# Kernel tuning notes

Hardware: AMD Instinct MI355X
Metric: run time of the kernel (lower is better)

## Reference

```python
import jax, jax.numpy as jnp
import numpy as np

B, S, H, NH = 2, 2048, 1024, 16
HD = H // NH  # head_dim = 64


def setup_inputs() -> dict:
    key = jax.random.key(0)
    kx, kl, kq, kk, kv, ko = jax.random.split(key, 6)
    scale = 1.0 / np.sqrt(H)
    return {
        "x": jax.random.normal(kx, (B, S, H), dtype=jnp.float32),
        "seq_lengths": jax.random.randint(kl, (B,), 1, S + 1, dtype=jnp.int32),
        "Wq": jax.random.normal(kq, (H, H), dtype=jnp.float32) * scale,
        "Wk": jax.random.normal(kk, (H, H), dtype=jnp.float32) * scale,
        "Wv": jax.random.normal(kv, (H, H), dtype=jnp.float32) * scale,
        "Wo": jax.random.normal(ko, (H, H), dtype=jnp.float32) * scale,
    }


def reference(x, seq_lengths, Wq, Wk, Wv, Wo):
    b, s, _ = x.shape
    # projections (nn.Linear with no bias: x @ W.T)
    q = (x @ Wq.T).reshape(b, s, NH, HD).transpose(0, 2, 1, 3)  # [b,h,s,d]
    k = (x @ Wk.T).reshape(b, s, NH, HD).transpose(0, 2, 1, 3)
    v = (x @ Wv.T).reshape(b, s, NH, HD).transpose(0, 2, 1, 3)

    scores = jnp.einsum("bhqd,bhkd->bhqk", q, k) / jnp.sqrt(jnp.float32(HD))

    causal = jnp.triu(jnp.ones((s, s), dtype=bool), k=1)[None, None]  # [1,1,s,s]
    padding = (jnp.arange(s)[None, :] >= seq_lengths[:, None])[:, None, None, :]
    mask = causal | padding
    scores = jnp.where(mask, -jnp.inf, scores)

    att = jax.nn.softmax(scores, axis=-1)  # stable: subtract row max once
    out = jnp.einsum("bhqk,bhkd->bhqd", att, v)
    out = out.transpose(0, 2, 1, 3).reshape(b, s, H)
    return out @ Wo.T
```

## Files before the change

### kernel.cpp

```cpp
#include <hip/hip_runtime.h>

typedef unsigned short u16;
typedef short bf16x8 __attribute__((ext_vector_type(8)));
typedef float f32x4 __attribute__((ext_vector_type(4)));

#define DEVINL __device__ __forceinline__

DEVINL u16 f2bf(float f) {
    union { float f; unsigned int u; } x;
    x.f = f;
    unsigned int u = x.u;
    unsigned int r = (u + 0x7fffu + ((u >> 16) & 1u)) >> 16;
    return (u16)r;
}

DEVINL u16 f2bf_fast(float f) {
    union { float f; unsigned int u; } x;
    x.f = f;
    return (u16)((x.u + 0x8000u) >> 16);
}

DEVINL void async16(const u16* g, u16* l) {
    __builtin_amdgcn_global_load_lds(
        (const __attribute__((address_space(1))) void*)g,
        (__attribute__((address_space(3))) void*)l, 16, 0, 0);
}

DEVINL void store_out(u16* p, float v)   { *p = f2bf(v); }
DEVINL void store_out(float* p, float v) { *p = v; }

__global__ void pma_cvt_kernel(const float* __restrict__ in, u16* __restrict__ out, int n4) {
    int i = blockIdx.x * blockDim.x + threadIdx.x;
    if (i < n4) {
        float4 v = reinterpret_cast<const float4*>(in)[i];
        ushort4 o;
        o.x = f2bf(v.x); o.y = f2bf(v.y); o.z = f2bf(v.z); o.w = f2bf(v.w);
        reinterpret_cast<ushort4*>(out)[i] = o;
    }
}

__global__ void pma_cvt4_kernel(const float* __restrict__ w0, const float* __restrict__ w1,
                                const float* __restrict__ w2, const float* __restrict__ w3,
                                u16* __restrict__ dst) {
    const int wsel = blockIdx.y;
    const float* in = (wsel == 0) ? w0 : (wsel == 1) ? w1 : (wsel == 2) ? w2 : w3;
    u16* out = dst + (size_t)wsel * 1024 * 1024;
    const float s = (wsel == 0) ? 0.125f : 1.0f;
    int i = blockIdx.x * blockDim.x + threadIdx.x;
    float4 v = reinterpret_cast<const float4*>(in)[i];
    ushort4 o;
    o.x = f2bf(v.x * s); o.y = f2bf(v.y * s); o.z = f2bf(v.z * s); o.w = f2bf(v.w * s);
    reinterpret_cast<ushort4*>(out)[i] = o;
}

template <typename OutT>
__global__ __launch_bounds__(256) void pma_gemm_bt(
    const u16* __restrict__ A,
    const u16* __restrict__ W0, const u16* __restrict__ W1, const u16* __restrict__ W2,
    OutT* __restrict__ O0, OutT* __restrict__ O1, OutT* __restrict__ O2,
    int K, int nbn_per, int vtr_which,
    const int* __restrict__ seq_lengths, int skip_kv)
{
    const int t = threadIdx.x;
    const int lane = t & 63, wave = t >> 6;
    const int m0 = blockIdx.x * 128;
    const int bn = blockIdx.y;
    const int which = bn / nbn_per;
    const int n0 = (bn % nbn_per) * 128;

    if (skip_kv && which != 0) {
        if ((m0 & 2047) >= seq_lengths[m0 >> 11]) return;
    }

    const u16* W = (which == 0) ? W0 : (which == 1) ? W1 : W2;
    OutT* O = (which == 0) ? O0 : (which == 1) ? O1 : O2;

    __shared__ u16 Alds[128 * 32];
    __shared__ u16 Blds[128 * 32];

    const int wm = wave >> 1, wn = wave & 1;
    const int r16 = lane & 15, g4 = lane >> 4;

    f32x4 acc[4][4];
    const f32x4 z = {0.f, 0.f, 0.f, 0.f};
#pragma unroll
    for (int m = 0; m < 4; ++m)
#pragma unroll
        for (int n = 0; n < 4; ++n) acc[m][n] = z;

    for (int k0 = 0; k0 < K; k0 += 32) {
        __syncthreads();
#pragma unroll
        for (int j = 0; j < 2; ++j) {
            int i = j * 256 + t;
            int row = i >> 2, seg = i & 3;
            async16(A + (size_t)(m0 + row) * K + k0 + seg * 8,
                    Alds + (size_t)(j * 256 + wave * 64) * 8);
            async16(W + (size_t)(n0 + row) * K + k0 + seg * 8,
                    Blds + (size_t)(j * 256 + wave * 64) * 8);
        }
        __syncthreads();

        bf16x8 af[4], bfr[4];
#pragma unroll
        for (int m = 0; m < 4; ++m)
            af[m] = *reinterpret_cast<const bf16x8*>(Alds + (wm * 64 + m * 16 + r16) * 32 + g4 * 8);
#pragma unroll
        for (int n = 0; n < 4; ++n)
            bfr[n] = *reinterpret_cast<const bf16x8*>(Blds + (wn * 64 + n * 16 + r16) * 32 + g4 * 8);
#pragma unroll
        for (int m = 0; m < 4; ++m)
#pragma unroll
            for (int n = 0; n < 4; ++n)
                acc[m][n] = __builtin_amdgcn_mfma_f32_16x16x32_bf16(af[m], bfr[n], acc[m][n], 0, 0, 0);
    }

    bool vtr = false;
    if constexpr (sizeof(OutT) == 2) vtr = (which == vtr_which);
    if (vtr) {
        if constexpr (sizeof(OutT) == 2) {
#pragma unroll
            for (int m = 0; m < 4; ++m)
#pragma unroll
                for (int n = 0; n < 4; ++n) {
                    int row = m0 + wm * 64 + m * 16 + g4 * 4;
                    int col = n0 + wn * 64 + n * 16 + r16;
                    ushort4 pk;
                    pk.x = f2bf(acc[m][n][0]); pk.y = f2bf(acc[m][n][1]);
                    pk.z = f2bf(acc[m][n][2]); pk.w = f2bf(acc[m][n][3]);
                    size_t addr = ((size_t)((row >> 11) * 16 + (col >> 6)) * 64 + (col & 63)) * 2048
                                  + (row & 2047);
                    *reinterpret_cast<ushort4*>((u16*)O + addr) = pk;
                }
        }
    } else {
#pragma unroll
        for (int m = 0; m < 4; ++m)
#pragma unroll
            for (int n = 0; n < 4; ++n) {
                int row = m0 + wm * 64 + m * 16 + g4 * 4;
                int col = n0 + wn * 64 + n * 16 + r16;
#pragma unroll
                for (int r = 0; r < 4; ++r)
                    store_out(&O[(size_t)(row + r) * 1024 + col], acc[m][n][r]);
            }
    }
}

__global__ __launch_bounds__(256, 4) void pma_attn_kernel(
    const u16* __restrict__ Q, const u16* __restrict__ Kp, const u16* __restrict__ Vt,
    const int* __restrict__ seq_lengths, u16* __restrict__ O)
{
    const int bx = blockIdx.x;
    const int qt = 31 - (bx >> 5);
    const int bh = bx & 31;
    const int h  = bh & 15;
    const int b  = bh >> 4;
    const int q0 = qt * 64;
    const int t = threadIdx.x, lane = t & 63, w = t >> 6;
    const int r16 = lane & 15, g4 = lane >> 4;
    const int seqlen = seq_lengths[b];
    const float L2E = 1.4426950408889634f;

    __shared__ u16 Klds[2 * 64 * 64];
    __shared__ u16 Vlds[2 * 64 * 64];
    __shared__ u16 Plds[64 * 64];

    const size_t bbase = (size_t)b * 2048 * 1024;
    const size_t hoff = (size_t)h * 64;
    const size_t vrow0 = (size_t)((b * 16 + h) * 64);

    const f32x4 z = {0.f, 0.f, 0.f, 0.f};
    const int krel = t >> 3;
    const int seg  = t & 7;

    const size_t qrowbase = bbase + (size_t)(q0 + w * 16 + r16) * 1024 + hoff;
    const bf16x8 qf0 = *reinterpret_cast<const bf16x8*>(Q + qrowbase + g4 * 8);
    const bf16x8 qf1 = *reinterpret_cast<const bf16x8*>(Q + qrowbase + 32 + g4 * 8);

    f32x4 acc[4];
#pragma unroll
    for (int f = 0; f < 4; ++f) acc[f] = z;
    float mrow = -1e30f, lrow = 0.f;

    int kmax = q0 + 63;
    if (seqlen - 1 < kmax) kmax = seqlen - 1;
    const int nt = (kmax >> 6) + 1;

    const u16* kbase = Kp + bbase + hoff + (size_t)krel * 1024 + seg * 8;
    const u16* vbase = Vt + (vrow0 + krel) * 2048 + seg * 8;
    const int stw = krel * 64 + ((seg ^ (krel & 7)) * 8);

    const int r7 = r16 & 7;
    const int kread_lo = r16 * 64 + ((g4 ^ r7) * 8);
    const int kread_hi = r16 * 64 + (((g4 + 4) ^ r7) * 8);
    const int prow = (w * 16 + r16) * 64;

    bf16x8 kreg[2], vreg[2];

#pragma unroll
    for (int j = 0; j < 2; ++j) {
        kreg[j] = *reinterpret_cast<const bf16x8*>(kbase + j * 32 * 1024);
        vreg[j] = *reinterpret_cast<const bf16x8*>(vbase + j * 32 * 2048);
    }
#pragma unroll
    for (int j = 0; j < 2; ++j) {
        *reinterpret_cast<bf16x8*>(Klds + stw + j * 2048) = kreg[j];
        *reinterpret_cast<bf16x8*>(Vlds + stw + j * 2048) = vreg[j];
    }
    __syncthreads();

    const int qhat = q0 + w * 16 + r16;

    for (int tt = 0; tt < nt; ++tt) {
        const int t0 = tt << 6;
        const int dbo = (tt & 1) << 12;
        const int dbn = 4096 - dbo;

        if (tt + 1 < nt) {
            const int t0n = (tt + 1) << 6;
#pragma unroll
            for (int j = 0; j < 2; ++j) {
                kreg[j] = *reinterpret_cast<const bf16x8*>(kbase + (size_t)t0n * 1024 + j * 32 * 1024);
                vreg[j] = *reinterpret_cast<const bf16x8*>(vbase + t0n + j * 32 * 2048);
            }
        }

        f32x4 sraw[4];
        __builtin_amdgcn_s_setprio(1);
#pragma unroll
        for (int kc = 0; kc < 4; ++kc) {
            bf16x8 kf0 = *reinterpret_cast<const bf16x8*>(Klds + dbo + kc * 1024 + kread_lo);
            bf16x8 kf1 = *reinterpret_cast<const bf16x8*>(Klds + dbo + kc * 1024 + kread_hi);
            f32x4 s = z;
            s = __builtin_amdgcn_mfma_f32_16x16x32_bf16(kf0, qf0, s, 0, 0, 0);
            s = __builtin_amdgcn_mfma_f32_16x16x32_bf16(kf1, qf1, s, 0, 0, 0);
            sraw[kc] = s;
        }
        __builtin_amdgcn_s_setprio(0);

        float sc[4][4];
        const bool needmask = (t0 == q0) || (t0 + 64 > seqlen);
        if (needmask) {
#pragma unroll
            for (int kc = 0; kc < 4; ++kc) {
                const int keyb = t0 + kc * 16 + g4 * 4;
#pragma unroll
                for (int r = 0; r < 4; ++r)
                    sc[kc][r] = ((keyb + r > qhat) || (keyb + r >= seqlen)) ? -1e30f : sraw[kc][r];
            }
        } else {
#pragma unroll
            for (int kc = 0; kc < 4; ++kc)
#pragma unroll
                for (int r = 0; r < 4; ++r) sc[kc][r] = sraw[kc][r];
        }

        float mx;
        {
            float m0 = fmaxf(fmaxf(sc[0][0], sc[0][1]), fmaxf(sc[0][2], sc[0][3]));
            float m1 = fmaxf(fmaxf(sc[1][0], sc[1][1]), fmaxf(sc[1][2], sc[1][3]));
            float m2 = fmaxf(fmaxf(sc[2][0], sc[2][1]), fmaxf(sc[2][2], sc[2][3]));
            float m3 = fmaxf(fmaxf(sc[3][0], sc[3][1]), fmaxf(sc[3][2], sc[3][3]));
            mx = fmaxf(fmaxf(m0, m1), fmaxf(m2, m3));
        }
        mx = fmaxf(mx, __shfl_xor(mx, 16, 64));
        mx = fmaxf(mx, __shfl_xor(mx, 32, 64));

        const bool norescale = __all(mx <= mrow + 8.0f);
        float mnew, corr;
        if (norescale) { mnew = mrow; corr = 1.0f; }
        else           { mnew = fmaxf(mrow, mx); corr = exp2f((mrow - mnew) * L2E); }

        const float nb = mnew * L2E;
#pragma unroll
        for (int kc = 0; kc < 4; ++kc)
#pragma unroll
            for (int r = 0; r < 4; ++r)
                sc[kc][r] = exp2f(__builtin_fmaf(sc[kc][r], L2E, -nb));
        float rs;
        {
            float s0 = (sc[0][0] + sc[0][1]) + (sc[0][2] + sc[0][3]);
            float s1 = (sc[1][0] + sc[1][1]) + (sc[1][2] + sc[1][3]);
            float s2 = (sc[2][0] + sc[2][1]) + (sc[2][2] + sc[2][3]);
            float s3 = (sc[3][0] + sc[3][1]) + (sc[3][2] + sc[3][3]);
            rs = (s0 + s1) + (s2 + s3);
        }
        rs += __shfl_xor(rs, 16, 64);
        rs += __shfl_xor(rs, 32, 64);
        lrow = lrow * corr + rs;
        mrow = mnew;

#pragma unroll
        for (int kc = 0; kc < 4; ++kc) {
            ushort4 pk;
            pk.x = f2bf_fast(sc[kc][0]); pk.y = f2bf_fast(sc[kc][1]);
            pk.z = f2bf_fast(sc[kc][2]); pk.w = f2bf_fast(sc[kc][3]);
            const int phys16 = (kc * 2 + (g4 >> 1)) ^ r7;
            *reinterpret_cast<ushort4*>(Plds + prow + phys16 * 8 + (g4 & 1) * 4) = pk;
        }

        if (!norescale) {
            float cr0 = __shfl(corr, g4 * 4 + 0, 64);
            float cr1 = __shfl(corr, g4 * 4 + 1, 64);
            float cr2 = __shfl(corr, g4 * 4 + 2, 64);
            float cr3 = __shfl(corr, g4 * 4 + 3, 64);
#pragma unroll
            for (int f = 0; f < 4; ++f) {
                f32x4 a = acc[f];
                a[0] *= cr0; a[1] *= cr1; a[2] *= cr2; a[3] *= cr3;
                acc[f] = a;
            }
        }

        __builtin_amdgcn_s_setprio(1);
#pragma unroll
        for (int kc2 = 0; kc2 < 2; ++kc2) {
            bf16x8 pa = *reinterpret_cast<const bf16x8*>(Plds + prow + (((kc2 * 4 + g4) ^ r7) * 8));
#pragma unroll
            for (int f = 0; f < 4; ++f) {
                bf16x8 vb = *reinterpret_cast<const bf16x8*>(
                    Vlds + dbo + (f * 16 + r16) * 64 + (((kc2 * 4 + g4) ^ r7) * 8));
                acc[f] = __builtin_amdgcn_mfma_f32_16x16x32_bf16(pa, vb, acc[f], 0, 0, 0);
            }
        }
        __builtin_amdgcn_s_setprio(0);

        if (tt + 1 < nt) {
#pragma unroll
            for (int j = 0; j < 2; ++j) {
                *reinterpret_cast<bf16x8*>(Klds + dbn + stw + j * 2048) = kreg[j];
                *reinterpret_cast<bf16x8*>(Vlds + dbn + stw + j * 2048) = vreg[j];
            }
            __syncthreads();
        }
    }

    {
        float lr0 = __shfl(lrow, g4 * 4 + 0, 64);
        float lr1 = __shfl(lrow, g4 * 4 + 1, 64);
        float lr2 = __shfl(lrow, g4 * 4 + 2, 64);
        float lr3 = __shfl(lrow, g4 * 4 + 3, 64);
        float lr[4] = {lr0, lr1, lr2, lr3};
#pragma unroll
        for (int f = 0; f < 4; ++f)
#pragma unroll
            for (int r = 0; r < 4; ++r) {
                int sr = q0 + w * 16 + g4 * 4 + r;
                float o = acc[f][r] / lr[r];
                O[bbase + (size_t)sr * 1024 + hoff + f * 16 + r16] = f2bf(o);
            }
    }
}

extern "C" void kernel_launch(void* const* d_in, const int* in_sizes, int n_in,
                              void* d_out, int out_size, void* d_ws, size_t ws_size,
                              hipStream_t stream) {
    const float* x   = (const float*)d_in[0];
    const int*   sql = (const int*)d_in[1];
    const float* Wq  = (const float*)d_in[2];
    const float* Wk  = (const float*)d_in[3];
    const float* Wv  = (const float*)d_in[4];
    const float* Wo  = (const float*)d_in[5];
    float* out = (float*)d_out;

    const size_t MB = 1024 * 1024;
    char* ws = (char*)d_ws;
    u16* xb   = (u16*)(ws + 0 * MB);
    u16* wqb  = (u16*)(ws + 8 * MB);
    u16* wkb  = (u16*)(ws + 10 * MB);
    u16* wvb  = (u16*)(ws + 12 * MB);
    u16* wob  = (u16*)(ws + 14 * MB);
    u16* Qb   = (u16*)(ws + 16 * MB);
    u16* Kb   = (u16*)(ws + 24 * MB);
    u16* Vtb  = (u16*)(ws + 32 * MB);
    u16* attb = (u16*)(ws + 40 * MB);

    pma_cvt_kernel<<<4096, 256, 0, stream>>>(x, xb, 1048576);
    pma_cvt4_kernel<<<dim3(1024, 4), 256, 0, stream>>>(Wq, Wk, Wv, Wo, wqb);

    pma_gemm_bt<u16><<<dim3(32, 24), 256, 0, stream>>>(xb, wqb, wkb, wvb, Qb, Kb, Vtb,
                                                       1024, 8, 2, sql, 1);

    pma_attn_kernel<<<1024, 256, 0, stream>>>(Qb, Kb, Vtb, sql, attb);

    pma_gemm_bt<float><<<dim3(32, 8), 256, 0, stream>>>(attb, wob, wob, wob, out, out, out,
                                                        1024, 8, -1, sql, 0);
}
```

Before: 120.8 us.

## Split GEMM into specialized QKV and output kernels with swizzled K=64 tiles

New measurement: 121.6 us. No clear change (+0.7%).

```diff
diff --git a/kernel.cpp b/kernel.cpp
--- a/kernel.cpp
+++ b/kernel.cpp
@@ -26,8 +26,9 @@
         (__attribute__((address_space(3))) void*)l, 16, 0, 0);
 }
 
-DEVINL void store_out(u16* p, float v)   { *p = f2bf(v); }
-DEVINL void store_out(float* p, float v) { *p = v; }
+DEVINL f32x4 mfma32(bf16x8 a, bf16x8 b, f32x4 c) {
+    return __builtin_amdgcn_mfma_f32_16x16x32_bf16(a, b, c, 0, 0, 0);
+}
 
 __global__ void pma_cvt_kernel(const float* __restrict__ in, u16* __restrict__ out, int n4) {
     int i = blockIdx.x * blockDim.x + threadIdx.x;
@@ -53,33 +54,29 @@
     reinterpret_cast<ushort4*>(out)[i] = o;
 }
 
-template <typename OutT>
-__global__ __launch_bounds__(256) void pma_gemm_bt(
+__global__ __launch_bounds__(256) void pma_gemm_qkv(
     const u16* __restrict__ A,
     const u16* __restrict__ W0, const u16* __restrict__ W1, const u16* __restrict__ W2,
-    OutT* __restrict__ O0, OutT* __restrict__ O1, OutT* __restrict__ O2,
-    int K, int nbn_per, int vtr_which,
-    const int* __restrict__ seq_lengths, int skip_kv)
+    u16* __restrict__ O0, u16* __restrict__ O1, u16* __restrict__ Vt,
+    const int* __restrict__ seq_lengths)
 {
     const int t = threadIdx.x;
     const int lane = t & 63, wave = t >> 6;
     const int m0 = blockIdx.x * 128;
     const int bn = blockIdx.y;
-    const int which = bn / nbn_per;
-    const int n0 = (bn % nbn_per) * 128;
-
-    if (skip_kv && which != 0) {
-        if ((m0 & 2047) >= seq_lengths[m0 >> 11]) return;
-    }
+    const int which = bn >> 3;
+    const int n0 = (bn & 7) * 128;
+
+    if (which != 0 && (m0 & 2047) >= seq_lengths[m0 >> 11]) return;
 
     const u16* W = (which == 0) ? W0 : (which == 1) ? W1 : W2;
-    OutT* O = (which == 0) ? O0 : (which == 1) ? O1 : O2;
-
-    __shared__ u16 Alds[128 * 32];
-    __shared__ u16 Blds[128 * 32];
+
+    __shared__ u16 Alds[128 * 64];
+    __shared__ u16 Blds[128 * 64];
 
     const int wm = wave >> 1, wn = wave & 1;
     const int r16 = lane & 15, g4 = lane >> 4;
+    const int r7 = r16 & 7;
 
     f32x4 acc[4][4];
     const f32x4 z = {0.f, 0.f, 0.f, 0.f};
@@ -88,63 +85,128 @@
 #pragma unroll
         for (int n = 0; n < 4; ++n) acc[m][n] = z;
 
-    for (int k0 = 0; k0 < K; k0 += 32) {
+    for (int k0 = 0; k0 < 1024; k0 += 64) {
         __syncthreads();
+#pragma unroll
+        for (int j = 0; j < 4; ++j) {
+            int i = j * 256 + t;
+            int row = i >> 3, seg = i & 7;
+            int sc = ((seg ^ (row & 7)) * 8);
+            async16(A + (size_t)(m0 + row) * 1024 + k0 + sc,
+                    Alds + (size_t)(j * 256 + wave * 64) * 8);
+            async16(W + (size_t)(n0 + row) * 1024 + k0 + sc,
+                    Blds + (size_t)(j * 256 + wave * 64) * 8);
+        }
+        __syncthreads();
+
+#pragma unroll
+        for (int half = 0; half < 2; ++half) {
+            bf16x8 af[4], bfr[4];
+#pragma unroll
+            for (int m = 0; m < 4; ++m)
+                af[m] = *reinterpret_cast<const bf16x8*>(
+                    Alds + (wm * 64 + m * 16 + r16) * 64 + (((half * 4 + g4) ^ r7) * 8));
+#pragma unroll
+            for (int n = 0; n < 4; ++n)
+                bfr[n] = *reinterpret_cast<const bf16x8*>(
+                    Blds + (wn * 64 + n * 16 + r16) * 64 + (((half * 4 + g4) ^ r7) * 8));
+#pragma unroll
+            for (int m = 0; m < 4; ++m)
+#pragma unroll
+                for (int n = 0; n < 4; ++n)
+                    acc[m][n] = mfma32(af[m], bfr[n], acc[m][n]);
+        }
+    }
+
+    if (which == 2) {
+#pragma unroll
+        for (int m = 0; m < 4; ++m)
+#pragma unroll
+            for (int n = 0; n < 4; ++n) {
+                int row = m0 + wm * 64 + m * 16 + g4 * 4;
+                int col = n0 + wn * 64 + n * 16 + r16;
+                ushort4 pk;
+                pk.x = f2bf(acc[m][n][0]); pk.y = f2bf(acc[m][n][1]);
+                pk.z = f2bf(acc[m][n][2]); pk.w = f2bf(acc[m][n][3]);
+                size_t addr = ((size_t)((row >> 11) * 16 + (col >> 6)) * 64 + (col & 63)) * 2048
+                              + (row & 2047);
+                *reinterpret_cast<ushort4*>(Vt + addr) = pk;
+            }
+    } else {
+        u16* O = (which == 0) ? O0 : O1;
+#pragma unroll
+        for (int m = 0; m < 4; ++m)
+#pragma unroll
+            for (int n = 0; n < 4; ++n) {
+                int row = m0 + wm * 64 + m * 16 + g4 * 4;
+                int col = n0 + wn * 64 + n * 16 + r16;
+#pragma unroll
+                for (int r = 0; r < 4; ++r)
+                    O[(size_t)(row + r) * 1024 + col] = f2bf(acc[m][n][r]);
+            }
+    }
+}
+
+__global__ __launch_bounds__(256) void pma_gemm_wo(
+    const u16* __restrict__ A, const u16* __restrict__ W, float* __restrict__ O)
+{
+    const int t = threadIdx.x;
+    const int lane = t & 63, wave = t >> 6;
+    const int m0 = blockIdx.x * 64;
+    const int n0 = blockIdx.y * 128;
+
+    __shared__ u16 Alds[64 * 32];
+    __shared__ u16 Blds[128 * 32];
+
+    const int r16 = lane & 15, g4 = lane >> 4;
+
+    f32x4 acc[4][2];
+    const f32x4 z = {0.f, 0.f, 0.f, 0.f};
+#pragma unroll
+    for (int m = 0; m < 4; ++m) {
+        acc[m][0] = z; acc[m][1] = z;
+    }
+
+    for (int k0 = 0; k0 < 1024; k0 += 32) {
+        __syncthreads();
+        {
+            int row = t >> 2, seg = t & 3;
+            async16(A + (size_t)(m0 + row) * 1024 + k0 + seg * 8,
+                    Alds + (size_t)(wave * 64) * 8);
+        }
 #pragma unroll
         for (int j = 0; j < 2; ++j) {
             int i = j * 256 + t;
             int row = i >> 2, seg = i & 3;
-            async16(A + (size_t)(m0 + row) * K + k0 + seg * 8,
-                    Alds + (size_t)(j * 256 + wave * 64) * 8);
-            async16(W + (size_t)(n0 + row) * K + k0 + seg * 8,
+            async16(W + (size_t)(n0 + row) * 1024 + k0 + seg * 8,
                     Blds + (size_t)(j * 256 + wave * 64) * 8);
         }
         __syncthreads();
 
-        bf16x8 af[4], bfr[4];
+        bf16x8 af[4], bfr[2];
 #pragma unroll
         for (int m = 0; m < 4; ++m)
-            af[m] = *reinterpret_cast<const bf16x8*>(Alds + (wm * 64 + m * 16 + r16) * 32 + g4 * 8);
-#pragma unroll
-        for (int n = 0; n < 4; ++n)
-            bfr[n] = *reinterpret_cast<const bf16x8*>(Blds + (wn * 64 + n * 16 + r16) * 32 + g4 * 8);
+            af[m] = *reinterpret_cast<const bf16x8*>(Alds + (m * 16 + r16) * 32 + g4 * 8);
+#pragma unroll
+        for (int n = 0; n < 2; ++n)
+            bfr[n] = *reinterpret_cast<const bf16x8*>(Blds + (wave * 32 + n * 16 + r16) * 32 + g4 * 8);
 #pragma unroll
         for (int m = 0; m < 4; ++m)
 #pragma unroll
-            for (int n = 0; n < 4; ++n)
-                acc[m][n] = __builtin_amdgcn_mfma_f32_16x16x32_bf16(af[m], bfr[n], acc[m][n], 0, 0, 0);
-    }
-
-    bool vtr = false;
-    if constexpr (sizeof(OutT) == 2) vtr = (which == vtr_which);
-    if (vtr) {
-        if constexpr (sizeof(OutT) == 2) {
-#pragma unroll
-            for (int m = 0; m < 4; ++m)
-#pragma unroll
-                for (int n = 0; n < 4; ++n) {
-                    int row = m0 + wm * 64 + m * 16 + g4 * 4;
-                    int col = n0 + wn * 64 + n * 16 + r16;
-                    ushort4 pk;
-                    pk.x = f2bf(acc[m][n][0]); pk.y = f2bf(acc[m][n][1]);
-                    pk.z = f2bf(acc[m][n][2]); pk.w = f2bf(acc[m][n][3]);
-                    size_t addr = ((size_t)((row >> 11) * 16 + (col >> 6)) * 64 + (col & 63)) * 2048
-                                  + (row & 2047);
-                    *reinterpret_cast<ushort4*>((u16*)O + addr) = pk;
-                }
-        }
-    } else {
-#pragma unroll
-        for (int m = 0; m < 4; ++m)
-#pragma unroll
-            for (int n = 0; n < 4; ++n) {
-                int row = m0 + wm * 64 + m * 16 + g4 * 4;
-                int col = n0 + wn * 64 + n * 16 + r16;
-#pragma unroll
-                for (int r = 0; r < 4; ++r)
-                    store_out(&O[(size_t)(row + r) * 1024 + col], acc[m][n][r]);
-            }
-    }
+            for (int n = 0; n < 2; ++n)
+                acc[m][n] = mfma32(af[m], bfr[n], acc[m][n]);
+    }
+
+#pragma unroll
+    for (int m = 0; m < 4; ++m)
+#pragma unroll
+        for (int n = 0; n < 2; ++n) {
+            int row = m0 + m * 16 + g4 * 4;
+            int col = n0 + wave * 32 + n * 16 + r16;
+#pragma unroll
+            for (int r = 0; r < 4; ++r)
+                O[(size_t)(row + r) * 1024 + col] = acc[m][n][r];
+        }
 }
 
 __global__ __launch_bounds__(256, 4) void pma_attn_kernel(
@@ -233,8 +295,8 @@
             bf16x8 kf0 = *reinterpret_cast<const bf16x8*>(Klds + dbo + kc * 1024 + kread_lo);
             bf16x8 kf1 = *reinterpret_cast<const bf16x8*>(Klds + dbo + kc * 1024 + kread_hi);
             f32x4 s = z;
-            s = __builtin_amdgcn_mfma_f32_16x16x32_bf16(kf0, qf0, s, 0, 0, 0);
-            s = __builtin_amdgcn_mfma_f32_16x16x32_bf16(kf1, qf1, s, 0, 0, 0);
+            s = mfma32(kf0, qf0, s);
+            s = mfma32(kf1, qf1, s);
             sraw[kc] = s;
         }
         __builtin_amdgcn_s_setprio(0);
@@ -321,7 +383,7 @@
             for (int f = 0; f < 4; ++f) {
                 bf16x8 vb = *reinterpret_cast<const bf16x8*>(
                     Vlds + dbo + (f * 16 + r16) * 64 + (((kc2 * 4 + g4) ^ r7) * 8));
-                acc[f] = __builtin_amdgcn_mfma_f32_16x16x32_bf16(pa, vb, acc[f], 0, 0, 0);
+                acc[f] = mfma32(pa, vb, acc[f]);
             }
         }
         __builtin_amdgcn_s_setprio(0);
@@ -379,11 +441,9 @@
     pma_cvt_kernel<<<4096, 256, 0, stream>>>(x, xb, 1048576);
     pma_cvt4_kernel<<<dim3(1024, 4), 256, 0, stream>>>(Wq, Wk, Wv, Wo, wqb);
 
-    pma_gemm_bt<u16><<<dim3(32, 24), 256, 0, stream>>>(xb, wqb, wkb, wvb, Qb, Kb, Vtb,
-                                                       1024, 8, 2, sql, 1);
+    pma_gemm_qkv<<<dim3(32, 24), 256, 0, stream>>>(xb, wqb, wkb, wvb, Qb, Kb, Vtb, sql);
 
     pma_attn_kernel<<<1024, 256, 0, stream>>>(Qb, Kb, Vtb, sql, attb);
 
-    pma_gemm_bt<float><<<dim3(32, 8), 256, 0, stream>>>(attb, wob, wob, wob, out, out, out,
-                                                        1024, 8, -1, sql, 0);
-}
+    pma_gemm_wo<<<dim3(64, 8), 256, 0, stream>>>(attb, wob, out);
+}
```
